# Kernel optimization log

Measured on AMD Instinct MI355X. Metric: run time of the kernel, lower is better.

The kernel has to match this reference:

```python
import jax, jax.numpy as jnp
import numpy as np

HIDDEN_SIZE = 1152
OUTPUT_LENGTH = 256
POSITIONS_PAD_VALUE = -1
GRID = 64  # 64x64 patch grid -> seq_len 4096


def setup_inputs() -> dict:
    key = jax.random.key(0)
    k1, k2 = jax.random.split(key)
    B, S, H = 8, GRID * GRID, HIDDEN_SIZE
    hidden_states = jax.random.normal(k1, (B, S, H), dtype=jnp.float32)
    positions_xy = jax.random.randint(k2, (B, S, 2), 0, GRID, dtype=jnp.int32)
    return {"hidden_states": hidden_states, "positions_xy": positions_xy}


def _pool(hidden_states, positions_xy):
    B, S, H = hidden_states.shape
    L = OUTPUT_LENGTH
    k = int(np.sqrt(S // L))
    assert k * k * L == S
    root = float(np.sqrt(HIDDEN_SIZE))

    padding = jnp.all(positions_xy == POSITIONS_PAD_VALUE, axis=-1)      # [B,S]
    safe = jnp.maximum(positions_xy, 0)                                   # [B,S,2]
    max_x = jnp.max(safe[..., 0], axis=-1, keepdims=True) + 1            # [B,1]
    kern = safe // k                                                      # [B,S,2]
    flat = kern[..., 0] + (max_x // k) * kern[..., 1]                     # [B,S] bin id in [0,L)
    w = jnp.where(padding, 0.0, 1.0 / float(k * k))                       # [B,S]

    def pool_one(xb, idxb, wb):
        # scatter-mean: equivalent to one-hot(idx)^T @ x with 1/k^2 weights
        pooled = jax.ops.segment_sum(xb * wb[:, None], idxb, num_segments=L)  # [L,H]
        wsum = jax.ops.segment_sum(wb, idxb, num_segments=L)                  # [L]
        return pooled, wsum > 0

    pooled, mask = jax.vmap(pool_one)(hidden_states.astype(jnp.float32), flat, w)
    pooled = pooled.astype(hidden_states.dtype) * root
    return pooled, mask


def reference(hidden_states, positions_xy):
    pooled, mask = _pool(hidden_states, positions_xy)
    return (pooled, mask)
```

## Files before the change

### kernel.cpp

```cpp
#include <hip/hip_runtime.h>

#define HD 1152
#define SQ 4096
#define NB 256
#define BT 8
#define KK 4

__global__ void __launch_bounds__(256) k_pool(const int* __restrict__ pos,
                                              const float* __restrict__ hs,
                                              float* __restrict__ out,
                                              float* __restrict__ mask) {
    int bl = blockIdx.x;
    int b = bl >> 8;
    unsigned l = (unsigned)(bl & (NB - 1));
    int tid = threadIdx.x;
    int wv = tid >> 6, lane = tid & 63;

    __shared__ unsigned short list[SQ];
    __shared__ int wcnt[4];
    __shared__ int smax[4];

    const int tokbase = tid * 16;
    const int4* pp = (const int4*)(pos + (size_t)b * SQ * 2) + tid * 8;
    int4 q[8];
    #pragma unroll
    for (int j = 0; j < 8; ++j) q[j] = pp[j];

    int mx = 0;
    #pragma unroll
    for (int j = 0; j < 8; ++j) mx = max(mx, max(q[j].x, q[j].z));
    #pragma unroll
    for (int off = 32; off > 0; off >>= 1)
        mx = max(mx, __shfl_down(mx, off, 64));
    if (lane == 0) smax[wv] = mx;
    __syncthreads();
    const int mxq = (max(max(smax[0], smax[1]), max(smax[2], smax[3])) + 1) / KK;

    unsigned m16 = 0;
    #pragma unroll
    for (int j = 0; j < 8; ++j) {
        int x0 = q[j].x, y0 = q[j].y, x1 = q[j].z, y1 = q[j].w;
        unsigned f0 = (unsigned)((max(x0, 0) >> 2) + mxq * (max(y0, 0) >> 2));
        unsigned f1 = (unsigned)((max(x1, 0) >> 2) + mxq * (max(y1, 0) >> 2));
        bool p0 = (x0 == -1) && (y0 == -1);
        bool p1 = (x1 == -1) && (y1 == -1);
        if (!p0 && f0 == l) m16 |= 1u << (2 * j);
        if (!p1 && f1 == l) m16 |= 1u << (2 * j + 1);
    }
    int cnt = __popc(m16);

    int pre = cnt;
    #pragma unroll
    for (int off = 1; off < 64; off <<= 1) {
        int n = __shfl_up(pre, off, 64);
        if (lane >= off) pre += n;
    }
    if (lane == 63) wcnt[wv] = pre;
    int excl = pre - cnt;
    __syncthreads();

    int woff = 0;
    #pragma unroll
    for (int v = 0; v < 4; ++v) if (v < wv) woff += wcnt[v];
    int total = wcnt[0] + wcnt[1] + wcnt[2] + wcnt[3];

    int r = woff + excl;
    unsigned m = m16;
    while (m) {
        int j = __ffs(m) - 1;
        m &= m - 1;
        list[r++] = (unsigned short)(tokbase + j);
    }
    __syncthreads();

    float4 a0 = make_float4(0.f, 0.f, 0.f, 0.f);
    float4 a1 = make_float4(0.f, 0.f, 0.f, 0.f);
    const float* hb = hs + (size_t)b * SQ * HD;
    int i = 0;
    for (; i + 3 < total; i += 4) {
        const float4* r0 = (const float4*)(hb + (size_t)list[i]     * HD);
        const float4* r1 = (const float4*)(hb + (size_t)list[i + 1] * HD);
        const float4* r2 = (const float4*)(hb + (size_t)list[i + 2] * HD);
        const float4* r3 = (const float4*)(hb + (size_t)list[i + 3] * HD);
        float4 v0 = r0[tid], v1 = r1[tid], v2 = r2[tid], v3 = r3[tid];
        a0.x += v0.x + v1.x + v2.x + v3.x;
        a0.y += v0.y + v1.y + v2.y + v3.y;
        a0.z += v0.z + v1.z + v2.z + v3.z;
        a0.w += v0.w + v1.w + v2.w + v3.w;
        if (tid < HD / 4 - 256) {
            float4 u0 = r0[256 + tid], u1 = r1[256 + tid];
            float4 u2 = r2[256 + tid], u3 = r3[256 + tid];
            a1.x += u0.x + u1.x + u2.x + u3.x;
            a1.y += u0.y + u1.y + u2.y + u3.y;
            a1.z += u0.z + u1.z + u2.z + u3.z;
            a1.w += u0.w + u1.w + u2.w + u3.w;
        }
    }
    for (; i < total; ++i) {
        const float4* r0 = (const float4*)(hb + (size_t)list[i] * HD);
        float4 v0 = r0[tid];
        a0.x += v0.x; a0.y += v0.y; a0.z += v0.z; a0.w += v0.w;
        if (tid < HD / 4 - 256) {
            float4 u0 = r0[256 + tid];
            a1.x += u0.x; a1.y += u0.y; a1.z += u0.z; a1.w += u0.w;
        }
    }

    const float scale = 2.1213203435596424f;
    float4* o = (float4*)(out + (size_t)bl * HD);
    a0.x *= scale; a0.y *= scale; a0.z *= scale; a0.w *= scale;
    o[tid] = a0;
    if (tid < HD / 4 - 256) {
        a1.x *= scale; a1.y *= scale; a1.z *= scale; a1.w *= scale;
        o[256 + tid] = a1;
    }
    if (tid == 0) mask[bl] = (total > 0) ? 1.0f : 0.0f;
}

extern "C" void kernel_launch(void* const* d_in, const int* in_sizes, int n_in,
                              void* d_out, int out_size, void* d_ws, size_t ws_size,
                              hipStream_t stream) {
    const float* hs = (const float*)d_in[0];
    const int* pos = (const int*)d_in[1];
    float* out = (float*)d_out;
    float* mask = out + (size_t)BT * NB * HD;

    k_pool<<<BT * NB, 256, 0, stream>>>(pos, hs, out, mask);
}
```

Measured before the change: 32.41 us.

## Process two output bins per 512-thread block to share position scan

Each block now handles two adjacent bins with 512 threads, scanning the batch's positions once and building both bins' token lists via a packed 16-bit dual prefix sum. Each 256-thread half then gathers and sums the rows for its own bin. The aim is to halve the redundant per-block position loading, max reduction and compaction work that each bin repeated. In exchange the grid has half as many blocks, each larger, and the counts share one packed 32-bit word per thread.

```diff
diff --git a/kernel.cpp b/kernel.cpp
--- a/kernel.cpp
+++ b/kernel.cpp
@@ -6,115 +6,136 @@
 #define BT 8
 #define KK 4
 
-__global__ void __launch_bounds__(256) k_pool(const int* __restrict__ pos,
-                                              const float* __restrict__ hs,
-                                              float* __restrict__ out,
-                                              float* __restrict__ mask) {
-    int bl = blockIdx.x;
-    int b = bl >> 8;
-    unsigned l = (unsigned)(bl & (NB - 1));
-    int tid = threadIdx.x;
-    int wv = tid >> 6, lane = tid & 63;
+__global__ void __launch_bounds__(512, 8) k_pool(const int* __restrict__ pos,
+                                                 const float* __restrict__ hs,
+                                                 float* __restrict__ out,
+                                                 float* __restrict__ mask) {
+    const int bl = blockIdx.x;
+    const int b = bl >> 7;
+    const unsigned la = (unsigned)((bl & 127) * 2);
+    const int tid = threadIdx.x;
+    const int wv = tid >> 6, lane = tid & 63;
 
     __shared__ unsigned short list[SQ];
-    __shared__ int wcnt[4];
-    __shared__ int smax[4];
+    __shared__ unsigned wsum[8];
+    __shared__ int smax[8];
 
-    const int tokbase = tid * 16;
-    const int4* pp = (const int4*)(pos + (size_t)b * SQ * 2) + tid * 8;
-    int4 q[8];
+    const int tokbase = tid * 8;
+    const int4* pp = (const int4*)(pos + (size_t)b * SQ * 2) + tid * 4;
+    int4 q[4];
     #pragma unroll
-    for (int j = 0; j < 8; ++j) q[j] = pp[j];
+    for (int j = 0; j < 4; ++j) q[j] = pp[j];
 
-    int mx = 0;
+    int mx = -1;
     #pragma unroll
-    for (int j = 0; j < 8; ++j) mx = max(mx, max(q[j].x, q[j].z));
+    for (int j = 0; j < 4; ++j) mx = max(mx, max(q[j].x, q[j].z));
     #pragma unroll
     for (int off = 32; off > 0; off >>= 1)
         mx = max(mx, __shfl_down(mx, off, 64));
     if (lane == 0) smax[wv] = mx;
     __syncthreads();
-    const int mxq = (max(max(smax[0], smax[1]), max(smax[2], smax[3])) + 1) / KK;
+    int mxa = smax[0];
+    #pragma unroll
+    for (int w = 1; w < 8; ++w) mxa = max(mxa, smax[w]);
+    const int mxq = (mxa + 1) / KK;
 
-    unsigned m16 = 0;
+    unsigned mA = 0, mB = 0;
     #pragma unroll
-    for (int j = 0; j < 8; ++j) {
+    for (int j = 0; j < 4; ++j) {
         int x0 = q[j].x, y0 = q[j].y, x1 = q[j].z, y1 = q[j].w;
         unsigned f0 = (unsigned)((max(x0, 0) >> 2) + mxq * (max(y0, 0) >> 2));
         unsigned f1 = (unsigned)((max(x1, 0) >> 2) + mxq * (max(y1, 0) >> 2));
         bool p0 = (x0 == -1) && (y0 == -1);
         bool p1 = (x1 == -1) && (y1 == -1);
-        if (!p0 && f0 == l) m16 |= 1u << (2 * j);
-        if (!p1 && f1 == l) m16 |= 1u << (2 * j + 1);
+        if (!p0) {
+            if (f0 == la)     mA |= 1u << (2 * j);
+            if (f0 == la + 1) mB |= 1u << (2 * j);
+        }
+        if (!p1) {
+            if (f1 == la)     mA |= 1u << (2 * j + 1);
+            if (f1 == la + 1) mB |= 1u << (2 * j + 1);
+        }
     }
-    int cnt = __popc(m16);
+    const unsigned cntP = (unsigned)__popc(mA) | ((unsigned)__popc(mB) << 16);
 
-    int pre = cnt;
+    unsigned pre = cntP;
     #pragma unroll
     for (int off = 1; off < 64; off <<= 1) {
-        int n = __shfl_up(pre, off, 64);
+        unsigned n = (unsigned)__shfl_up((int)pre, off, 64);
         if (lane >= off) pre += n;
     }
-    if (lane == 63) wcnt[wv] = pre;
-    int excl = pre - cnt;
+    if (lane == 63) wsum[wv] = pre;
     __syncthreads();
 
-    int woff = 0;
+    unsigned woff = 0, tot = 0;
     #pragma unroll
-    for (int v = 0; v < 4; ++v) if (v < wv) woff += wcnt[v];
-    int total = wcnt[0] + wcnt[1] + wcnt[2] + wcnt[3];
+    for (int w = 0; w < 8; ++w) {
+        unsigned v = wsum[w];
+        if (w < wv) woff += v;
+        tot += v;
+    }
+    const unsigned exclP = woff + pre - cntP;
+    const int totalA = (int)(tot & 0xFFFFu);
+    const int totalB = (int)(tot >> 16);
 
-    int r = woff + excl;
-    unsigned m = m16;
-    while (m) {
-        int j = __ffs(m) - 1;
-        m &= m - 1;
-        list[r++] = (unsigned short)(tokbase + j);
+    {
+        int r = (int)(exclP & 0xFFFFu);
+        unsigned m = mA;
+        while (m) { int j = __ffs(m) - 1; m &= m - 1; list[r++] = (unsigned short)(tokbase + j); }
+        r = totalA + (int)(exclP >> 16);
+        m = mB;
+        while (m) { int j = __ffs(m) - 1; m &= m - 1; list[r++] = (unsigned short)(tokbase + j); }
     }
     __syncthreads();
 
+    const int half = tid >> 8;
+    const int t = tid & 255;
+    const unsigned short* lst = list + (half ? totalA : 0);
+    const int cnt = half ? totalB : totalA;
+    const float* hb = hs + (size_t)b * SQ * HD;
+
     float4 a0 = make_float4(0.f, 0.f, 0.f, 0.f);
     float4 a1 = make_float4(0.f, 0.f, 0.f, 0.f);
-    const float* hb = hs + (size_t)b * SQ * HD;
     int i = 0;
-    for (; i + 3 < total; i += 4) {
-        const float4* r0 = (const float4*)(hb + (size_t)list[i]     * HD);
-        const float4* r1 = (const float4*)(hb + (size_t)list[i + 1] * HD);
-        const float4* r2 = (const float4*)(hb + (size_t)list[i + 2] * HD);
-        const float4* r3 = (const float4*)(hb + (size_t)list[i + 3] * HD);
-        float4 v0 = r0[tid], v1 = r1[tid], v2 = r2[tid], v3 = r3[tid];
+    for (; i + 3 < cnt; i += 4) {
+        const float4* r0 = (const float4*)(hb + (size_t)lst[i]     * HD);
+        const float4* r1 = (const float4*)(hb + (size_t)lst[i + 1] * HD);
+        const float4* r2 = (const float4*)(hb + (size_t)lst[i + 2] * HD);
+        const float4* r3 = (const float4*)(hb + (size_t)lst[i + 3] * HD);
+        float4 v0 = r0[t], v1 = r1[t], v2 = r2[t], v3 = r3[t];
         a0.x += v0.x + v1.x + v2.x + v3.x;
         a0.y += v0.y + v1.y + v2.y + v3.y;
         a0.z += v0.z + v1.z + v2.z + v3.z;
         a0.w += v0.w + v1.w + v2.w + v3.w;
-        if (tid < HD / 4 - 256) {
-            float4 u0 = r0[256 + tid], u1 = r1[256 + tid];
-            float4 u2 = r2[256 + tid], u3 = r3[256 + tid];
+        if (t < HD / 4 - 256) {
+            float4 u0 = r0[256 + t], u1 = r1[256 + t];
+            float4 u2 = r2[256 + t], u3 = r3[256 + t];
             a1.x += u0.x + u1.x + u2.x + u3.x;
             a1.y += u0.y + u1.y + u2.y + u3.y;
             a1.z += u0.z + u1.z + u2.z + u3.z;
             a1.w += u0.w + u1.w + u2.w + u3.w;
         }
     }
-    for (; i < total; ++i) {
-        const float4* r0 = (const float4*)(hb + (size_t)list[i] * HD);
-        float4 v0 = r0[tid];
+    for (; i < cnt; ++i) {
+        const float4* r0 = (const float4*)(hb + (size_t)lst[i] * HD);
+        float4 v0 = r0[t];
         a0.x += v0.x; a0.y += v0.y; a0.z += v0.z; a0.w += v0.w;
-        if (tid < HD / 4 - 256) {
-            float4 u0 = r0[256 + tid];
+        if (t < HD / 4 - 256) {
+            float4 u0 = r0[256 + t];
             a1.x += u0.x; a1.y += u0.y; a1.z += u0.z; a1.w += u0.w;
         }
     }
 
     const float scale = 2.1213203435596424f;
-    float4* o = (float4*)(out + (size_t)bl * HD);
+    const int orow = (b << 8) + (int)la + half;
+    float4* o = (float4*)(out + (size_t)orow * HD);
     a0.x *= scale; a0.y *= scale; a0.z *= scale; a0.w *= scale;
-    o[tid] = a0;
-    if (tid < HD / 4 - 256) {
+    o[t] = a0;
+    if (t < HD / 4 - 256) {
         a1.x *= scale; a1.y *= scale; a1.z *= scale; a1.w *= scale;
-        o[256 + tid] = a1;
+        o[256 + t] = a1;
     }
-    if (tid == 0) mask[bl] = (total > 0) ? 1.0f : 0.0f;
+    if (t == 0) mask[orow] = (cnt > 0) ? 1.0f : 0.0f;
 }
 
 extern "C" void kernel_launch(void* const* d_in, const int* in_sizes, int n_in,
@@ -125,5 +146,5 @@
     float* out = (float*)d_out;
     float* mask = out + (size_t)BT * NB * HD;
 
-    k_pool<<<BT * NB, 256, 0, stream>>>(pos, hs, out, mask);
+    k_pool<<<BT * NB / 2, 512, 0, stream>>>(pos, hs, out, mask);
 }
```

Result: slower. 38.35 us (+18.3%).
